# Kernel tuning notes

Hardware: AMD Instinct MI355X
Metric: run time of the kernel (lower is better)

## Reference

```python
import jax, jax.numpy as jnp
import numpy as np

FP8_E4M3_MAX = 448.0

def fp8_quant_dequant(x):
    # Per-tensor dynamic scaling to e4m3 range, round-trip through fp8.
    amax = jnp.max(jnp.abs(x))
    scale = FP8_E4M3_MAX / jnp.maximum(amax, 1e-12)
    xq = (x * scale).astype(jnp.float8_e4m3fn).astype(x.dtype) / scale
    return xq

def fp8_linear(x, w, b):
    # quantize activations and weights to fp8, GEMM in the compute dtype, add bias
    return jnp.matmul(fp8_quant_dequant(x), fp8_quant_dequant(w)) + b

def setup_inputs() -> dict:
    key = jax.random.key(0)
    k1, k2, k3 = jax.random.split(key, 3)
    M, D_IN, D_H, D_OUT = 8192, 4096, 16384, 4096
    x = jax.random.normal(k1, (M, D_IN), dtype=jnp.float32)
    w1 = jax.random.normal(k2, (D_IN, D_H), dtype=jnp.float32)
    b1 = jnp.zeros((D_H,), dtype=jnp.float32)
    w2 = jax.random.normal(k3, (D_H, D_OUT), dtype=jnp.float32)
    b2 = jnp.zeros((D_OUT,), dtype=jnp.float32)
    return {"x": x, "w1": w1, "b1": b1, "w2": w2, "b2": b2}

def reference(x, w1, b1, w2, b2):
    h = jax.nn.relu(fp8_linear(x, w1, b1))
    return fp8_linear(h, w2, b2)
```

## Files before the change

kernel.cpp:

```cpp
#include <hip/hip_runtime.h>
#include <stdint.h>

typedef float f32x4 __attribute__((ext_vector_type(4)));
typedef int v4i __attribute__((ext_vector_type(4)));
typedef int v8i __attribute__((ext_vector_type(8)));

#define FP8MAX 448.0f

__device__ __forceinline__ float amax_scale(float amax) {
    return FP8MAX / fmaxf(amax, 1e-12f);
}

__global__ void amax_kernel(const float* __restrict__ x, long n, float* __restrict__ out) {
    long idx = (long)blockIdx.x * blockDim.x + threadIdx.x;
    long stride = (long)gridDim.x * blockDim.x;
    float m = 0.0f;
    for (long j = idx * 4; j < n; j += stride * 4) {
        f32x4 v = *(const f32x4*)(x + j);
        m = fmaxf(m, fmaxf(fmaxf(__builtin_fabsf(v.x), __builtin_fabsf(v.y)),
                           fmaxf(__builtin_fabsf(v.z), __builtin_fabsf(v.w))));
    }
#pragma unroll
    for (int o = 32; o > 0; o >>= 1) m = fmaxf(m, __shfl_xor(m, o, 64));
    if ((threadIdx.x & 63) == 0) atomicMax((int*)out, __float_as_int(m));
}

__global__ void quant_kernel(const float* __restrict__ x, uint8_t* __restrict__ q,
                             const float* __restrict__ amaxp, long n) {
    const float s = amax_scale(*amaxp);
    long idx = (long)blockIdx.x * blockDim.x + threadIdx.x;
    long stride = (long)gridDim.x * blockDim.x;
    for (long j = idx * 4; j < n; j += stride * 4) {
        f32x4 v = *(const f32x4*)(x + j);
        int p0 = __builtin_amdgcn_cvt_pk_fp8_f32(v.x * s, v.y * s, 0, false);
        int p1 = __builtin_amdgcn_cvt_pk_fp8_f32(v.z * s, v.w * s, 0, false);
        *(uint32_t*)(q + j) = (uint32_t)(p0 & 0xffff) | ((uint32_t)p1 << 16);
    }
}

__global__ void quant_transpose_kernel(const float* __restrict__ w, uint8_t* __restrict__ wqT,
                                       const float* __restrict__ amaxp, int R, int C) {
    __shared__ float tile[32][33];
    const float sc = amax_scale(*amaxp);
    const int col0 = blockIdx.x * 32;
    const int row0 = blockIdx.y * 32;
    const int tx = threadIdx.x & 31;
    const int ty = threadIdx.x >> 5;
#pragma unroll
    for (int i = 0; i < 4; i++)
        tile[ty + i * 8][tx] = w[(long)(row0 + ty + i * 8) * C + col0 + tx];
    __syncthreads();
    const int c  = threadIdx.x >> 3;
    const int kk = (threadIdx.x & 7) * 4;
    float v0 = tile[kk + 0][c] * sc, v1 = tile[kk + 1][c] * sc;
    float v2 = tile[kk + 2][c] * sc, v3 = tile[kk + 3][c] * sc;
    int p0 = __builtin_amdgcn_cvt_pk_fp8_f32(v0, v1, 0, false);
    int p1 = __builtin_amdgcn_cvt_pk_fp8_f32(v2, v3, 0, false);
    *(uint32_t*)(wqT + (long)(col0 + c) * R + row0 + kk) =
        (uint32_t)(p0 & 0xffff) | ((uint32_t)p1 << 16);
}

__device__ __forceinline__ void lds_dma16(const void* g, void* l) {
    __builtin_amdgcn_global_load_lds((__attribute__((address_space(1))) void*)(void*)g,
                                     (__attribute__((address_space(3))) void*)l, 16, 0, 0);
}

template <bool RELU, bool AMAX>
__global__ __launch_bounds__(256) void gemm_mxfp8_kernel(
    const uint8_t* __restrict__ A, const uint8_t* __restrict__ Bt,
    float* __restrict__ C, const float* __restrict__ bias,
    const float* __restrict__ amaxA, const float* __restrict__ amaxB,
    float* __restrict__ amaxOut, int M, int N, int K) {
    __shared__ __align__(16) uint8_t As[128 * 128];
    __shared__ __align__(16) uint8_t Bs[128 * 128];
    const int t = threadIdx.x;
    const int lane = t & 63;
    const int wave = t >> 6;
    const int bm = blockIdx.x, bn = blockIdx.y;

    const int rs = t >> 3;
    const int us = (t & 7) ^ (rs & 7);
    const uint8_t* ag = A + (long)(bm * 128 + rs) * K + us * 16;
    const uint8_t* bg = Bt + (long)(bn * 128 + rs) * K + us * 16;
    uint8_t* asd = As + t * 16;
    uint8_t* bsd = Bs + t * 16;
    const long dstep = (long)32 * K;

    f32x4 acc[4][4] = {};

    const int wm = wave & 1, wn = wave >> 1;
    const int lrow = lane & 15;
    const int g = lane >> 4;
    const int x7 = lane & 7;
    const int roA = (wm * 64 + lrow) * 128;
    const int roB = (wn * 64 + lrow) * 128;
    const int u0 = ((2 * g + 0) ^ x7) * 16;
    const int u1 = ((2 * g + 1) ^ x7) * 16;

    for (int k0 = 0; k0 < K; k0 += 128) {
        __syncthreads();
#pragma unroll
        for (int d = 0; d < 4; d++) {
            lds_dma16(ag + d * dstep, asd + d * 4096);
            lds_dma16(bg + d * dstep, bsd + d * 4096);
        }
        ag += 128; bg += 128;
        __syncthreads();
        v8i af[4], bf[4];
#pragma unroll
        for (int i = 0; i < 4; i++) {
            const int ro = roA + i * 16 * 128;
            *(v4i*)&af[i] = *(const v4i*)(As + ro + u0);
            *((v4i*)&af[i] + 1) = *(const v4i*)(As + ro + u1);
        }
#pragma unroll
        for (int j = 0; j < 4; j++) {
            const int ro = roB + j * 16 * 128;
            *(v4i*)&bf[j] = *(const v4i*)(Bs + ro + u0);
            *((v4i*)&bf[j] + 1) = *(const v4i*)(Bs + ro + u1);
        }
#pragma unroll
        for (int i = 0; i < 4; i++)
#pragma unroll
            for (int j = 0; j < 4; j++)
                acc[i][j] = __builtin_amdgcn_mfma_scale_f32_16x16x128_f8f6f4(
                    af[i], bf[j], acc[i][j], 0, 0,
                    0, 0x7f7f7f7f, 0, 0x7f7f7f7f);
    }

    const float inv = 1.0f / (amax_scale(*amaxA) * amax_scale(*amaxB));
    const int rg = (lane >> 4) * 4;
    const int cl = lane & 15;
    const int orow = bm * 128 + wm * 64 + rg;
    const int ocol = bn * 128 + wn * 64 + cl;
    float lmax = 0.0f;
#pragma unroll
    for (int j = 0; j < 4; j++) {
        const float bv = bias[ocol + j * 16];
#pragma unroll
        for (int i = 0; i < 4; i++) {
#pragma unroll
            for (int r = 0; r < 4; r++) {
                float v = acc[i][j][r] * inv + bv;
                if (RELU) v = fmaxf(v, 0.0f);
                C[(long)(orow + i * 16 + r) * N + ocol + j * 16] = v;
                if (AMAX) lmax = fmaxf(lmax, __builtin_fabsf(v));
            }
        }
    }
    if (AMAX) {
#pragma unroll
        for (int o = 32; o > 0; o >>= 1) lmax = fmaxf(lmax, __shfl_xor(lmax, o, 64));
        if (lane == 0) atomicMax((int*)amaxOut, __float_as_int(lmax));
    }
}

extern "C" void kernel_launch(void* const* d_in, const int* in_sizes, int n_in,
                              void* d_out, int out_size, void* d_ws, size_t ws_size,
                              hipStream_t stream) {
    const float* x  = (const float*)d_in[0];
    const float* w1 = (const float*)d_in[1];
    const float* b1 = (const float*)d_in[2];
    const float* w2 = (const float*)d_in[3];
    const float* b2 = (const float*)d_in[4];
    float* out = (float*)d_out;

    const int N1 = in_sizes[2];
    const int N2 = in_sizes[4];
    const int K1 = in_sizes[1] / N1;
    const int M  = in_sizes[0] / K1;

    uint8_t* ws = (uint8_t*)d_ws;
    float* amax_x  = (float*)(ws + 0);
    float* amax_w1 = (float*)(ws + 4);
    float* amax_w2 = (float*)(ws + 8);
    float* amax_h  = (float*)(ws + 12);
    size_t off = 256;
    uint8_t* xq   = ws + off; off += (size_t)M * K1;
    uint8_t* w1qT = ws + off; off += (size_t)K1 * N1;
    uint8_t* w2qT = ws + off; off += (size_t)N1 * N2;
    uint8_t* hq   = ws + off; off += (size_t)M * N1;
    float*   h    = (float*)(ws + off); off += (size_t)M * N1 * 4;

    hipMemsetAsync(d_ws, 0, 256, stream);

    amax_kernel<<<1024, 256, 0, stream>>>(x,  (long)M * K1,  amax_x);
    amax_kernel<<<1024, 256, 0, stream>>>(w1, (long)K1 * N1, amax_w1);
    amax_kernel<<<1024, 256, 0, stream>>>(w2, (long)N1 * N2, amax_w2);

    quant_kernel<<<2048, 256, 0, stream>>>(x, xq, amax_x, (long)M * K1);
    quant_transpose_kernel<<<dim3(N1 / 32, K1 / 32), 256, 0, stream>>>(w1, w1qT, amax_w1, K1, N1);
    quant_transpose_kernel<<<dim3(N2 / 32, N1 / 32), 256, 0, stream>>>(w2, w2qT, amax_w2, N1, N2);

    gemm_mxfp8_kernel<true, true><<<dim3(M / 128, N1 / 128), 256, 0, stream>>>(
        xq, w1qT, h, b1, amax_x, amax_w1, amax_h, M, N1, K1);

    quant_kernel<<<4096, 256, 0, stream>>>(h, hq, amax_h, (long)M * N1);

    gemm_mxfp8_kernel<false, false><<<dim3(M / 128, N2 / 128), 256, 0, stream>>>(
        hq, w2qT, out, b2, amax_h, amax_w2, nullptr, M, N2, N1);
}
```

Baseline: 2.206 ms.

## Enlarge GEMM tiles to 256x256 with double-buffered LDS and swizzled block order

The FP8 GEMM moves from 128x128 tiles with 4 waves to 256x256 tiles with 8 waves. Each wave now computes 128x64. The next K-slice is loaded into a second LDS buffer while the current one feeds MFMAs, with barriers and s_setprio interleaving the loads and the math. Block IDs are remapped to improve L2 reuse across neighbouring tiles. This is meant to cut global traffic per FLOP and hide load latency, at the cost of 128KB of LDS, more accumulator registers, and lower occupancy. The launch_bounds(512,2) may not be satisfiable with that much LDS.

```diff
diff --git a/kernel.cpp b/kernel.cpp
--- a/kernel.cpp
+++ b/kernel.cpp
@@ -66,79 +66,112 @@
 }
 
 template <bool RELU, bool AMAX>
-__global__ __launch_bounds__(256) void gemm_mxfp8_kernel(
+__global__ __launch_bounds__(512, 2) void gemm_mxfp8_kernel(
     const uint8_t* __restrict__ A, const uint8_t* __restrict__ Bt,
     float* __restrict__ C, const float* __restrict__ bias,
     const float* __restrict__ amaxA, const float* __restrict__ amaxB,
     float* __restrict__ amaxOut, int M, int N, int K) {
-    __shared__ __align__(16) uint8_t As[128 * 128];
-    __shared__ __align__(16) uint8_t Bs[128 * 128];
+    __shared__ __align__(16) uint8_t As[2][256 * 128];
+    __shared__ __align__(16) uint8_t Bs[2][256 * 128];
+
     const int t = threadIdx.x;
     const int lane = t & 63;
     const int wave = t >> 6;
-    const int bm = blockIdx.x, bn = blockIdx.y;
+    const int wm = wave >> 2;
+    const int wn = wave & 3;
+
+    int bid = (int)blockIdx.x;
+    bid = (bid & 7) * ((int)gridDim.x >> 3) + (bid >> 3);
+    const int nbn = N >> 8;
+    const int bm = bid / nbn;
+    const int bn = bid - bm * nbn;
 
     const int rs = t >> 3;
     const int us = (t & 7) ^ (rs & 7);
-    const uint8_t* ag = A + (long)(bm * 128 + rs) * K + us * 16;
-    const uint8_t* bg = Bt + (long)(bn * 128 + rs) * K + us * 16;
-    uint8_t* asd = As + t * 16;
-    uint8_t* bsd = Bs + t * 16;
-    const long dstep = (long)32 * K;
-
-    f32x4 acc[4][4] = {};
-
-    const int wm = wave & 1, wn = wave >> 1;
+    const uint8_t* ag = A + (long)(bm * 256 + rs) * K + us * 16;
+    const uint8_t* bg = Bt + (long)(bn * 256 + rs) * K + us * 16;
+
+    auto stage = [&](int buf, int kt) {
+        const uint8_t* a_ = ag + (long)kt * 128;
+        const uint8_t* b_ = bg + (long)kt * 128;
+        uint8_t* al_ = &As[buf][t * 16];
+        uint8_t* bl_ = &Bs[buf][t * 16];
+#pragma unroll
+        for (int d = 0; d < 4; d++) {
+            lds_dma16(a_ + (long)d * 64 * K, al_ + d * 8192);
+            lds_dma16(b_ + (long)d * 64 * K, bl_ + d * 8192);
+        }
+    };
+
     const int lrow = lane & 15;
     const int g = lane >> 4;
     const int x7 = lane & 7;
-    const int roA = (wm * 64 + lrow) * 128;
-    const int roB = (wn * 64 + lrow) * 128;
     const int u0 = ((2 * g + 0) ^ x7) * 16;
     const int u1 = ((2 * g + 1) ^ x7) * 16;
-
-    for (int k0 = 0; k0 < K; k0 += 128) {
-        __syncthreads();
-#pragma unroll
-        for (int d = 0; d < 4; d++) {
-            lds_dma16(ag + d * dstep, asd + d * 4096);
-            lds_dma16(bg + d * dstep, bsd + d * 4096);
-        }
-        ag += 128; bg += 128;
-        __syncthreads();
-        v8i af[4], bf[4];
-#pragma unroll
-        for (int i = 0; i < 4; i++) {
-            const int ro = roA + i * 16 * 128;
-            *(v4i*)&af[i] = *(const v4i*)(As + ro + u0);
-            *((v4i*)&af[i] + 1) = *(const v4i*)(As + ro + u1);
-        }
+    const int roA = (wm * 128 + lrow) * 128;
+    const int roB = (wn * 64 + lrow) * 128;
+
+    f32x4 acc[8][4] = {};
+    const int NT = K >> 7;
+
+    stage(0, 0);
+    asm volatile("s_waitcnt vmcnt(0)" ::: "memory");
+    __builtin_amdgcn_s_barrier();
+    asm volatile("" ::: "memory");
+
+    for (int kt = 0; kt < NT; ++kt) {
+        const int b = kt & 1;
+        const uint8_t* Ab = As[b];
+        const uint8_t* Bb = Bs[b];
+        if (kt + 1 < NT) stage(b ^ 1, kt + 1);
+
+        v8i bf[4];
 #pragma unroll
         for (int j = 0; j < 4; j++) {
-            const int ro = roB + j * 16 * 128;
-            *(v4i*)&bf[j] = *(const v4i*)(Bs + ro + u0);
-            *((v4i*)&bf[j] + 1) = *(const v4i*)(Bs + ro + u1);
-        }
-#pragma unroll
-        for (int i = 0; i < 4; i++)
-#pragma unroll
-            for (int j = 0; j < 4; j++)
-                acc[i][j] = __builtin_amdgcn_mfma_scale_f32_16x16x128_f8f6f4(
-                    af[i], bf[j], acc[i][j], 0, 0,
+            const uint8_t* p = Bb + roB + j * 2048;
+            *(v4i*)&bf[j] = *(const v4i*)(p + u0);
+            *((v4i*)&bf[j] + 1) = *(const v4i*)(p + u1);
+        }
+#pragma unroll
+        for (int ph = 0; ph < 4; ph++) {
+            v8i a0, a1;
+            const uint8_t* pa0 = Ab + roA + (2 * ph + 0) * 2048;
+            const uint8_t* pa1 = Ab + roA + (2 * ph + 1) * 2048;
+            *(v4i*)&a0 = *(const v4i*)(pa0 + u0);
+            *((v4i*)&a0 + 1) = *(const v4i*)(pa0 + u1);
+            *(v4i*)&a1 = *(const v4i*)(pa1 + u0);
+            *((v4i*)&a1 + 1) = *(const v4i*)(pa1 + u1);
+            __builtin_amdgcn_s_barrier();
+            __builtin_amdgcn_s_setprio(1);
+#pragma unroll
+            for (int j = 0; j < 4; j++) {
+                acc[2 * ph + 0][j] = __builtin_amdgcn_mfma_scale_f32_16x16x128_f8f6f4(
+                    a0, bf[j], acc[2 * ph + 0][j], 0, 0,
                     0, 0x7f7f7f7f, 0, 0x7f7f7f7f);
+                acc[2 * ph + 1][j] = __builtin_amdgcn_mfma_scale_f32_16x16x128_f8f6f4(
+                    a1, bf[j], acc[2 * ph + 1][j], 0, 0,
+                    0, 0x7f7f7f7f, 0, 0x7f7f7f7f);
+            }
+            __builtin_amdgcn_s_setprio(0);
+            if (ph == 3) {
+                asm volatile("s_waitcnt vmcnt(0)" ::: "memory");
+            }
+            __builtin_amdgcn_s_barrier();
+            if (ph == 3) asm volatile("" ::: "memory");
+        }
     }
 
     const float inv = 1.0f / (amax_scale(*amaxA) * amax_scale(*amaxB));
     const int rg = (lane >> 4) * 4;
     const int cl = lane & 15;
-    const int orow = bm * 128 + wm * 64 + rg;
-    const int ocol = bn * 128 + wn * 64 + cl;
+    const int orow = bm * 256 + wm * 128 + rg;
+    const int ocol = bn * 256 + wn * 64 + cl;
     float lmax = 0.0f;
 #pragma unroll
     for (int j = 0; j < 4; j++) {
         const float bv = bias[ocol + j * 16];
 #pragma unroll
-        for (int i = 0; i < 4; i++) {
+        for (int i = 0; i < 8; i++) {
 #pragma unroll
             for (int r = 0; r < 4; r++) {
                 float v = acc[i][j][r] * inv + bv;
@@ -192,11 +225,11 @@
     quant_transpose_kernel<<<dim3(N1 / 32, K1 / 32), 256, 0, stream>>>(w1, w1qT, amax_w1, K1, N1);
     quant_transpose_kernel<<<dim3(N2 / 32, N1 / 32), 256, 0, stream>>>(w2, w2qT, amax_w2, N1, N2);
 
-    gemm_mxfp8_kernel<true, true><<<dim3(M / 128, N1 / 128), 256, 0, stream>>>(
+    gemm_mxfp8_kernel<true, true><<<(M / 256) * (N1 / 256), 512, 0, stream>>>(
         xq, w1qT, h, b1, amax_x, amax_w1, amax_h, M, N1, K1);
 
     quant_kernel<<<4096, 256, 0, stream>>>(h, hq, amax_h, (long)M * N1);
 
-    gemm_mxfp8_kernel<false, false><<<dim3(M / 128, N2 / 128), 256, 0, stream>>>(
+    gemm_mxfp8_kernel<false, false><<<(M / 256) * (N2 / 256), 512, 0, stream>>>(
         hq, w2qT, out, b2, amax_h, amax_w2, nullptr, M, N2, N1);
 }
```

Result: slower. 2.582 ms (+17.1%).

## Double-buffer LDS tiles in FP8 GEMM and remap blocks across XCDs

Applied to the files above, without the earlier changes.

The GEMM kernel now keeps two LDS buffers per operand. It issues the global-to-LDS DMA for the next K tile before running the MFMAs on the current one, and needs only one wait and barrier per iteration instead of two syncthreads with a serial load. This is meant to hide global load latency behind compute. It also permutes the linear block index so that consecutive tiles are spread in strides across the eight XCDs, aiming for better L2 reuse. The cost is doubled LDS per block (64KB), which may lower occupancy.

```diff
diff --git a/kernel.cpp b/kernel.cpp
--- a/kernel.cpp
+++ b/kernel.cpp
@@ -71,20 +71,38 @@
     float* __restrict__ C, const float* __restrict__ bias,
     const float* __restrict__ amaxA, const float* __restrict__ amaxB,
     float* __restrict__ amaxOut, int M, int N, int K) {
-    __shared__ __align__(16) uint8_t As[128 * 128];
-    __shared__ __align__(16) uint8_t Bs[128 * 128];
+    __shared__ __align__(16) uint8_t As[2][128 * 128];
+    __shared__ __align__(16) uint8_t Bs[2][128 * 128];
     const int t = threadIdx.x;
     const int lane = t & 63;
     const int wave = t >> 6;
-    const int bm = blockIdx.x, bn = blockIdx.y;
+
+    {
+    }
+    const int gx = gridDim.x;
+    int lin = (int)blockIdx.y * gx + (int)blockIdx.x;
+    const int total = gx * (int)gridDim.y;
+    lin = (lin & 7) * (total >> 3) + (lin >> 3);
+    const int bm = lin % gx;
+    const int bn = lin / gx;
 
     const int rs = t >> 3;
     const int us = (t & 7) ^ (rs & 7);
     const uint8_t* ag = A + (long)(bm * 128 + rs) * K + us * 16;
     const uint8_t* bg = Bt + (long)(bn * 128 + rs) * K + us * 16;
-    uint8_t* asd = As + t * 16;
-    uint8_t* bsd = Bs + t * 16;
     const long dstep = (long)32 * K;
+
+    auto stage = [&](int buf, int kt) {
+        const uint8_t* a_ = ag + (long)kt * 128;
+        const uint8_t* b_ = bg + (long)kt * 128;
+        uint8_t* al = &As[buf][t * 16];
+        uint8_t* bl = &Bs[buf][t * 16];
+#pragma unroll
+        for (int d = 0; d < 4; d++) {
+            lds_dma16(a_ + d * dstep, al + d * 4096);
+            lds_dma16(b_ + d * dstep, bl + d * 4096);
+        }
+    };
 
     f32x4 acc[4][4] = {};
 
@@ -97,27 +115,32 @@
     const int u0 = ((2 * g + 0) ^ x7) * 16;
     const int u1 = ((2 * g + 1) ^ x7) * 16;
 
-    for (int k0 = 0; k0 < K; k0 += 128) {
-        __syncthreads();
-#pragma unroll
-        for (int d = 0; d < 4; d++) {
-            lds_dma16(ag + d * dstep, asd + d * 4096);
-            lds_dma16(bg + d * dstep, bsd + d * 4096);
-        }
-        ag += 128; bg += 128;
-        __syncthreads();
+    const int NT = K >> 7;
+
+    stage(0, 0);
+    asm volatile("s_waitcnt vmcnt(0)" ::: "memory");
+    __builtin_amdgcn_s_barrier();
+    asm volatile("" ::: "memory");
+
+    for (int kt = 0; kt < NT; ++kt) {
+        const int b = kt & 1;
+        if (kt + 1 < NT) stage(b ^ 1, kt + 1);
+        asm volatile("" ::: "memory");
+
+        const uint8_t* __restrict__ Ab = &As[b][0];
+        const uint8_t* __restrict__ Bb = &Bs[b][0];
         v8i af[4], bf[4];
 #pragma unroll
         for (int i = 0; i < 4; i++) {
-            const int ro = roA + i * 16 * 128;
-            *(v4i*)&af[i] = *(const v4i*)(As + ro + u0);
-            *((v4i*)&af[i] + 1) = *(const v4i*)(As + ro + u1);
+            const uint8_t* p = Ab + roA + i * 16 * 128;
+            *(v4i*)&af[i] = *(const v4i*)(p + u0);
+            *((v4i*)&af[i] + 1) = *(const v4i*)(p + u1);
         }
 #pragma unroll
         for (int j = 0; j < 4; j++) {
-            const int ro = roB + j * 16 * 128;
-            *(v4i*)&bf[j] = *(const v4i*)(Bs + ro + u0);
-            *((v4i*)&bf[j] + 1) = *(const v4i*)(Bs + ro + u1);
+            const uint8_t* p = Bb + roB + j * 16 * 128;
+            *(v4i*)&bf[j] = *(const v4i*)(p + u0);
+            *((v4i*)&bf[j] + 1) = *(const v4i*)(p + u1);
         }
 #pragma unroll
         for (int i = 0; i < 4; i++)
@@ -126,6 +149,9 @@
                 acc[i][j] = __builtin_amdgcn_mfma_scale_f32_16x16x128_f8f6f4(
                     af[i], bf[j], acc[i][j], 0, 0,
                     0, 0x7f7f7f7f, 0, 0x7f7f7f7f);
+        asm volatile("s_waitcnt vmcnt(0)" ::: "memory");
+        __builtin_amdgcn_s_barrier();
+        asm volatile("" ::: "memory");
     }
 
     const float inv = 1.0f / (amax_scale(*amaxA) * amax_scale(*amaxB));
```

Measured after the change: 2.743 ms. +24.4%, slower.
